# Performance work log

Hardware: AMD Instinct MI355X
Metric: run time of the kernel (lower is better)

## Reference

```python
import jax, jax.numpy as jnp
import numpy as np
import math

DIM = 1024
NUM_HEADS = 16
HEAD_DIM = DIM // NUM_HEADS
EPS = 1e-6
DILATED = 2
WINDOW = 2  # window_size init arg; actual window = L * WINDOW per side


def setup_inputs() -> dict:
    key = jax.random.key(0)
    ks = jax.random.split(key, 14)
    B, S = 1, 8704
    x = jax.random.normal(ks[0], (B, S, DIM), jnp.float32)
    ang = jax.random.uniform(ks[1], (S, HEAD_DIM // 2), jnp.float32, -jnp.pi, jnp.pi)
    freqs_cos = jnp.cos(ang)
    freqs_sin = jnp.sin(ang)
    def lin(k):
        return 0.02 * jax.random.normal(k, (DIM, DIM), jnp.float32)
    def bias(k):
        return 0.01 * jax.random.normal(k, (DIM,), jnp.float32)
    return {
        'x': x, 'freqs_cos': freqs_cos, 'freqs_sin': freqs_sin,
        'wq': lin(ks[2]), 'bq': bias(ks[3]),
        'wk': lin(ks[4]), 'bk': bias(ks[5]),
        'wv': lin(ks[6]), 'bv': bias(ks[7]),
        'wo': lin(ks[8]), 'bo': bias(ks[9]),
        'gq': 1.0 + 0.02 * jax.random.normal(ks[10], (DIM,), jnp.float32),
        'gk': 1.0 + 0.02 * jax.random.normal(ks[11], (DIM,), jnp.float32),
        'f': 34, 'L': 256,
    }


def rmsnorm(h, g):
    return h * jax.lax.rsqrt(jnp.mean(h * h, axis=-1, keepdims=True) + EPS) * g


def rope(h, cos, sin):
    # h: [B,S,D] viewed as interleaved complex pairs per head, rotated by unit freqs
    B, S, D = h.shape
    hp = h.reshape(B, S, NUM_HEADS, HEAD_DIM // 2, 2)
    a, b = hp[..., 0], hp[..., 1]
    c = cos[None, :, None, :]
    s = sin[None, :, None, :]
    ra = a * c - b * s
    rb = a * s + b * c
    return jnp.stack([ra, rb], axis=-1).reshape(B, S, D)


def windowed_attention(q, k, v, w):
    # sliding-window attention: query i attends keys j with |i-j| <= w (inclusive)
    B, S, D = q.shape
    H, hd = NUM_HEADS, HEAD_DIM
    def heads(t):
        return t.reshape(B, S, H, hd).transpose(0, 2, 1, 3)  # [B,H,S,hd]
    qh, kh, vh = heads(q), heads(k), heads(v)
    C = w  # block size == window -> only 3 neighbor key blocks per query block
    pad = (-S) % C
    Sp = S + pad
    nb = Sp // C
    def blocks(t):
        return jnp.pad(t, ((0, 0), (0, 0), (0, pad), (0, 0))).reshape(B, H, nb, C, hd)
    qb = blocks(qh)
    def win(t):
        tb = jnp.pad(blocks(t), ((0, 0), (0, 0), (1, 1), (0, 0), (0, 0)))
        return jnp.concatenate([tb[:, :, i:i + nb] for i in range(3)], axis=3)  # [B,H,nb,3C,hd]
    kw_, vw_ = win(kh), win(vh)
    scores = jnp.einsum('bhnqd,bhnkd->bhnqk', qb, kw_) * (1.0 / math.sqrt(hd))
    qi = jnp.arange(nb)[:, None, None] * C + jnp.arange(C)[None, :, None]      # [nb,C,1]
    kj = (jnp.arange(nb)[:, None, None] - 1) * C + jnp.arange(3 * C)[None, None, :]  # [nb,1,3C]
    valid = (kj >= 0) & (kj < S) & (qi - kj <= w) & (kj - qi <= w)
    scores = jnp.where(valid, scores, -1e9)
    p = jax.nn.softmax(scores, axis=-1)
    o = jnp.einsum('bhnqk,bhnkd->bhnqd', p, vw_)
    return o.reshape(B, H, Sp, hd)[:, :, :S].transpose(0, 2, 1, 3).reshape(B, S, D)


def reference(x, freqs_cos, freqs_sin, wq, bq, wk, bk, wv, bv, wo, bo, gq, gk, f, L):
    B, S, D = x.shape
    q = rope(rmsnorm(x @ wq + bq, gq), freqs_cos, freqs_sin)
    k = rope(rmsnorm(x @ wk + bk, gk), freqs_cos, freqs_sin)
    v = x @ wv + bv
    w = L * WINDOW
    use_dilated = DILATED > 1 and S // (DILATED * L) > 1
    if use_dilated:
        blk = DILATED * L
        pad_len = blk - S % blk  # == blk when S % blk == 0 (faithful to torch code)
        Sp = S + pad_len
        n = Sp // blk
        def padd(t):
            return jnp.pad(t, ((0, 0), (0, pad_len), (0, 0)))
        def dil(t):
            # 'b (n d l) c -> (b d) (n l) c'
            return t.reshape(B, n, DILATED, L, D).transpose(0, 2, 1, 3, 4).reshape(B * DILATED, n * L, D)
        q, k, v = dil(padd(q)), dil(padd(k)), dil(padd(v))
    o = windowed_attention(q, k, v, w)
    out = o @ wo + bo
    if use_dilated:
        # '(b d) (n l) c -> b (n d l) c', then drop pad
        out = out.reshape(B, DILATED, n, L, D).transpose(0, 2, 1, 3, 4).reshape(B, n * DILATED * L, D)
        out = out[:, :S]
    return out
```

## Files before the change

kernel.cpp:

```cpp
#include <hip/hip_runtime.h>
#include <hip/hip_bf16.h>
#include <stdint.h>

#define DIM 1024
#define NH 16
#define HD 64
#define S_ORIG 8704
#define WIN 512

typedef __attribute__((ext_vector_type(8))) short short8;
typedef __attribute__((ext_vector_type(4))) float f32x4;

__device__ __forceinline__ float bf2f(unsigned short u) {
    return __uint_as_float(((unsigned int)u) << 16);
}
__device__ __forceinline__ unsigned short f2bf(float f) {
    unsigned int x = __float_as_uint(f);
    unsigned int r = x + 0x7fffu + ((x >> 16) & 1u);
    return (unsigned short)(r >> 16);
}
__device__ __forceinline__ unsigned int pkbf(float a, float b) {
    unsigned int ua = (__float_as_uint(a) + 0x8000u) >> 16;
    unsigned int ub = (__float_as_uint(b) + 0x8000u) & 0xffff0000u;
    return ua | ub;
}

#define GLD_LDS(gptr, lptr) \
    __builtin_amdgcn_global_load_lds((const __attribute__((address_space(1))) void*)(gptr), \
                                     (__attribute__((address_space(3))) void*)(lptr), 16, 0, 0)

__global__ __launch_bounds__(256) void cvt_x(const float* __restrict__ x,
                                             unsigned short* __restrict__ xb) {
    int i = (blockIdx.x * 256 + threadIdx.x) * 4;
    float4 v = *(const float4*)(x + i);
    ushort4 o;
    o.x = f2bf(v.x); o.y = f2bf(v.y); o.z = f2bf(v.z); o.w = f2bf(v.w);
    *(ushort4*)(xb + i) = o;
}

__global__ __launch_bounds__(256) void transpose_w(const float* __restrict__ w0,
                                                   const float* __restrict__ w1,
                                                   const float* __restrict__ w2,
                                                   const float* __restrict__ w3,
                                                   unsigned short* __restrict__ wt) {
    __shared__ float ts[64][65];
    const int z = blockIdx.z;
    const float* w = z == 0 ? w0 : z == 1 ? w1 : z == 2 ? w2 : w3;
    unsigned short* o = wt + (size_t)z * DIM * DIM;
    const int kb = blockIdx.x * 64, nb = blockIdx.y * 64;
    const int t = threadIdx.x, c = t & 63, r4 = t >> 6;
#pragma unroll
    for (int rr = 0; rr < 16; rr++) {
        int row = rr * 4 + r4;
        ts[row][c] = w[(size_t)(kb + row) * DIM + nb + c];
    }
    __syncthreads();
#pragma unroll
    for (int rr = 0; rr < 16; rr++) {
        int nl = rr * 4 + r4;
        o[(size_t)(nb + nl) * DIM + kb + c] = f2bf(ts[c][nl]);
    }
}

template <int OUTF32>
__global__ __launch_bounds__(256) void gemm_bf16(const unsigned short* __restrict__ A,
                                                 const unsigned short* __restrict__ Bt,
                                                 const float* __restrict__ b0,
                                                 const float* __restrict__ b1,
                                                 const float* __restrict__ b2,
                                                 void* __restrict__ Cout) {
    __shared__ __align__(16) unsigned short As[128 * 32];
    __shared__ __align__(16) unsigned short Bs[128 * 32];
    const int z = blockIdx.z;
    const unsigned short* B = Bt + (size_t)z * DIM * DIM;
    const float* bias = z == 0 ? b0 : (z == 1 ? b1 : b2);
    const int m0 = blockIdx.y * 128, n0 = blockIdx.x * 128;
    const int tid = threadIdx.x;
    const int lane = tid & 63, wv = tid >> 6;
    const int wr = wv >> 1, wc = wv & 1;
    const int quad = lane >> 4, r = lane & 15;

    f32x4 acc[4][4];
#pragma unroll
    for (int i = 0; i < 4; i++)
#pragma unroll
        for (int j = 0; j < 4; j++)
#pragma unroll
            for (int t4 = 0; t4 < 4; t4++) acc[i][j][t4] = 0.0f;

    const unsigned short* a_base = A + (size_t)m0 * DIM;
    const unsigned short* b_base = B + (size_t)n0 * DIM;
    const int c0 = wv * 128 + lane;
    const int r0 = c0 >> 2, o0 = (c0 & 3) * 8;
    const int c1 = c0 + 64;
    const int r1 = c1 >> 2, o1 = (c1 & 3) * 8;
    unsigned short* lA0 = &As[(size_t)(wv * 128) * 8];
    unsigned short* lA1 = &As[(size_t)(wv * 128 + 64) * 8];
    unsigned short* lB0 = &Bs[(size_t)(wv * 128) * 8];
    unsigned short* lB1 = &Bs[(size_t)(wv * 128 + 64) * 8];

    for (int k0 = 0; k0 < DIM; k0 += 32) {
        __syncthreads();
        GLD_LDS(a_base + (size_t)r0 * DIM + k0 + o0, lA0);
        GLD_LDS(a_base + (size_t)r1 * DIM + k0 + o1, lA1);
        GLD_LDS(b_base + (size_t)r0 * DIM + k0 + o0, lB0);
        GLD_LDS(b_base + (size_t)r1 * DIM + k0 + o1, lB1);
        __syncthreads();
        short8 af[4], bfr[4];
#pragma unroll
        for (int i = 0; i < 4; i++)
            af[i] = *(const short8*)&As[(wr * 64 + i * 16 + r) * 32 + quad * 8];
#pragma unroll
        for (int j = 0; j < 4; j++)
            bfr[j] = *(const short8*)&Bs[(wc * 64 + j * 16 + r) * 32 + quad * 8];
#pragma unroll
        for (int i = 0; i < 4; i++)
#pragma unroll
            for (int j = 0; j < 4; j++)
                acc[i][j] = __builtin_amdgcn_mfma_f32_16x16x32_bf16(af[i], bfr[j], acc[i][j], 0, 0, 0);
    }

#pragma unroll
    for (int i = 0; i < 4; i++) {
        const int row = m0 + wr * 64 + i * 16 + quad * 4;
#pragma unroll
        for (int j = 0; j < 4; j++) {
            const int col = n0 + wc * 64 + j * 16 + r;
            const float bvl = bias[col];
#pragma unroll
            for (int t4 = 0; t4 < 4; t4++) {
                float vv = acc[i][j][t4] + bvl;
                if (OUTF32) {
                    ((float*)Cout)[(size_t)(row + t4) * DIM + col] = vv;
                } else {
                    ((unsigned short*)Cout)[(size_t)z * S_ORIG * DIM + (size_t)(row + t4) * DIM + col] = f2bf(vv);
                }
            }
        }
    }
}

__global__ __launch_bounds__(256) void norm_rope(unsigned short* __restrict__ hq,
                                                 unsigned short* __restrict__ hk,
                                                 const float* __restrict__ gq,
                                                 const float* __restrict__ gk,
                                                 const float* __restrict__ fcos,
                                                 const float* __restrict__ fsin) {
    const int srow = blockIdx.x;
    const int z = blockIdx.y;
    unsigned short* h = z == 0 ? hq : hk;
    const float* g = z == 0 ? gq : gk;
    const int tid = threadIdx.x;
    const int base = tid * 4;
    unsigned short* hp = h + (size_t)srow * DIM;

    ushort4 raw = *(const ushort4*)(hp + base);
    float v0 = bf2f(raw.x), v1 = bf2f(raw.y), v2 = bf2f(raw.z), v3 = bf2f(raw.w);
    float ss = v0 * v0 + v1 * v1 + v2 * v2 + v3 * v3;
#pragma unroll
    for (int off = 1; off < 64; off <<= 1) ss += __shfl_xor(ss, off, 64);
    __shared__ float red[4];
    if ((tid & 63) == 0) red[tid >> 6] = ss;
    __syncthreads();
    ss = red[0] + red[1] + red[2] + red[3];
    const float rinv = rsqrtf(ss * (1.0f / DIM) + 1e-6f);

    float4 gv = *(const float4*)(g + base);
    v0 *= rinv * gv.x;
    v1 *= rinv * gv.y;
    v2 *= rinv * gv.z;
    v3 *= rinv * gv.w;

    const int i0 = (base & 63) >> 1;
    float2 cs = *(const float2*)(fcos + (size_t)srow * 32 + i0);
    float2 sn = *(const float2*)(fsin + (size_t)srow * 32 + i0);
    float ra0 = v0 * cs.x - v1 * sn.x;
    float rb0 = v0 * sn.x + v1 * cs.x;
    float ra1 = v2 * cs.y - v3 * sn.y;
    float rb1 = v2 * sn.y + v3 * cs.y;
    ushort4 o;
    o.x = f2bf(ra0); o.y = f2bf(rb0); o.z = f2bf(ra1); o.w = f2bf(rb1);
    *(ushort4*)(hp + base) = o;
}

__global__ __launch_bounds__(256) void attn(const unsigned short* __restrict__ qkv,
                                            unsigned short* __restrict__ ob) {
    __shared__ __align__(16) unsigned short Ks[64 * 72];
    __shared__ __align__(16) unsigned short Vt[64 * 72];
    __shared__ __align__(16) unsigned short Ps[4][16 * 72];

    const int head = blockIdx.x >> 1;
    const int d = blockIdx.x & 1;
    const int qt = blockIdx.y;
    const int tid = threadIdx.x;
    const int lane = tid & 63, wv = tid >> 6;
    const int quad = lane >> 4, r16 = lane & 15;

    const unsigned short* qb = qkv;
    const unsigned short* kb = qkv + (size_t)S_ORIG * DIM;
    const unsigned short* vb = qkv + (size_t)2 * S_ORIG * DIM;

    const int qi = qt * 64 + wv * 16 + r16;
    const int og_q = ((qi >> 8) << 9) + d * 256 + (qi & 255);
    short8 qf[2];
    {
        const unsigned short* qrow = qb + (size_t)og_q * DIM + head * HD + quad * 8;
#pragma unroll
        for (int c = 0; c < 2; c++) {
            union { int4 i4; unsigned short u[8]; short8 s8; } in, outv;
            in.i4 = *(const int4*)(qrow + c * 32);
#pragma unroll
            for (int j = 0; j < 8; j++) outv.u[j] = f2bf(bf2f(in.u[j]) * 0.125f);
            qf[c] = outv.s8;
        }
    }

    f32x4 oacc[4];
    float lsum = 0.0f;
#pragma unroll
    for (int nt = 0; nt < 4; nt++)
#pragma unroll
        for (int rr = 0; rr < 4; rr++) oacc[nt][rr] = 0.0f;

    const int kt_lo = (qt - 8 > 0) ? (qt - 8) : 0;
    const int kt_hi = (qt + 8 < 67) ? (qt + 8) : 67;

    const int st_row0 = tid >> 3, st_ch = (tid & 7) * 8;
    const int vt_kk = (tid & 31) * 2, vt_d0 = (tid >> 5) * 8;

    for (int kt = kt_lo; kt <= kt_hi; kt++) {
        const int kbase = kt * 64;
        __syncthreads();

#pragma unroll
        for (int half = 0; half < 2; half++) {
            const int row = st_row0 + half * 32;
            const int kj = kbase + row;
            const int ok = ((kj >> 8) << 9) + d * 256 + (kj & 255);
            *(int4*)&Ks[row * 72 + st_ch] = *(const int4*)(kb + (size_t)ok * DIM + head * HD + st_ch);
        }
        {
            const int kj0 = kbase + vt_kk;
            const int ok0 = ((kj0 >> 8) << 9) + d * 256 + (kj0 & 255);
            union { int4 i4; unsigned short u[8]; } a0, a1;
            a0.i4 = *(const int4*)(vb + (size_t)ok0 * DIM + head * HD + vt_d0);
            a1.i4 = *(const int4*)(vb + (size_t)(ok0 + 1) * DIM + head * HD + vt_d0);
#pragma unroll
            for (int i = 0; i < 8; i++) {
                unsigned int pack = (unsigned int)a0.u[i] | ((unsigned int)a1.u[i] << 16);
                *(unsigned int*)&Vt[(vt_d0 + i) * 72 + vt_kk] = pack;
            }
        }
        __syncthreads();

        f32x4 sv[4];
#pragma unroll
        for (int nt = 0; nt < 4; nt++) {
            short8 k0f = *(const short8*)&Ks[(nt * 16 + r16) * 72 + quad * 8];
            short8 k1f = *(const short8*)&Ks[(nt * 16 + r16) * 72 + 32 + quad * 8];
            f32x4 a = {0.0f, 0.0f, 0.0f, 0.0f};
            a = __builtin_amdgcn_mfma_f32_16x16x32_bf16(k0f, qf[0], a, 0, 0, 0);
            a = __builtin_amdgcn_mfma_f32_16x16x32_bf16(k1f, qf[1], a, 0, 0, 0);
            sv[nt] = a;
        }

        const bool edge = (kt == qt - 8) || (kt == qt + 8);
        unsigned short* pw = &Ps[wv][0];
#pragma unroll
        for (int nt = 0; nt < 4; nt++) {
            float p[4];
#pragma unroll
            for (int rr = 0; rr < 4; rr++) {
                float e = __expf(sv[nt][rr]);
                if (edge) {
                    const int kj = kbase + nt * 16 + quad * 4 + rr;
                    const int dl = qi - kj;
                    if (dl > WIN || dl < -WIN) e = 0.0f;
                }
                p[rr] = e;
            }
            lsum += (p[0] + p[1]) + (p[2] + p[3]);
            uint2 pk;
            pk.x = pkbf(p[0], p[1]);
            pk.y = pkbf(p[2], p[3]);
            *(uint2*)&pw[r16 * 72 + nt * 16 + quad * 4] = pk;
        }
        __asm__ volatile("s_waitcnt lgkmcnt(0)" ::: "memory");

        short8 pf0 = *(const short8*)&pw[r16 * 72 + quad * 8];
        short8 pf1 = *(const short8*)&pw[r16 * 72 + 32 + quad * 8];
#pragma unroll
        for (int nt = 0; nt < 4; nt++) {
            short8 v0f = *(const short8*)&Vt[(nt * 16 + r16) * 72 + quad * 8];
            short8 v1f = *(const short8*)&Vt[(nt * 16 + r16) * 72 + 32 + quad * 8];
            oacc[nt] = __builtin_amdgcn_mfma_f32_16x16x32_bf16(v0f, pf0, oacc[nt], 0, 0, 0);
            oacc[nt] = __builtin_amdgcn_mfma_f32_16x16x32_bf16(v1f, pf1, oacc[nt], 0, 0, 0);
        }
    }

    lsum += __shfl_xor(lsum, 16, 64);
    lsum += __shfl_xor(lsum, 32, 64);
    {
        const int cnt = (qi + WIN < 4607 ? qi + WIN : 4607) - 4351;
        if (cnt > 0) lsum += (float)cnt;
    }
    const float linv = 1.0f / lsum;

#pragma unroll
    for (int nt = 0; nt < 4; nt++) {
        ushort4 o;
        o.x = f2bf(oacc[nt][0] * linv);
        o.y = f2bf(oacc[nt][1] * linv);
        o.z = f2bf(oacc[nt][2] * linv);
        o.w = f2bf(oacc[nt][3] * linv);
        *(ushort4*)&ob[(size_t)og_q * DIM + head * HD + nt * 16 + quad * 4] = o;
    }
}

extern "C" void kernel_launch(void* const* d_in, const int* in_sizes, int n_in,
                              void* d_out, int out_size, void* d_ws, size_t ws_size,
                              hipStream_t stream) {
    const float* x    = (const float*)d_in[0];
    const float* fcos = (const float*)d_in[1];
    const float* fsin = (const float*)d_in[2];
    const float* wq   = (const float*)d_in[3];
    const float* bq   = (const float*)d_in[4];
    const float* wk   = (const float*)d_in[5];
    const float* bk   = (const float*)d_in[6];
    const float* wv   = (const float*)d_in[7];
    const float* bv   = (const float*)d_in[8];
    const float* wo   = (const float*)d_in[9];
    const float* bo   = (const float*)d_in[10];
    const float* gq   = (const float*)d_in[11];
    const float* gk   = (const float*)d_in[12];

    char* ws = (char*)d_ws;
    unsigned short* xb = (unsigned short*)(ws);
    unsigned short* wt = (unsigned short*)(ws + 17825792);
    unsigned short* h  = (unsigned short*)(ws + 26214400);
    unsigned short* ob = (unsigned short*)(ws + 79691776);
    float* outp = (float*)d_out;

    cvt_x<<<8704, 256, 0, stream>>>(x, xb);
    transpose_w<<<dim3(16, 16, 4), 256, 0, stream>>>(wq, wk, wv, wo, wt);
    gemm_bf16<0><<<dim3(8, 68, 3), 256, 0, stream>>>(xb, wt, bq, bk, bv, (void*)h);
    norm_rope<<<dim3(8704, 2), 256, 0, stream>>>(h, h + (size_t)S_ORIG * DIM, gq, gk, fcos, fsin);
    attn<<<dim3(32, 68), 256, 0, stream>>>(h, ob);
    gemm_bf16<1><<<dim3(8, 68, 1), 256, 0, stream>>>(ob, wt + (size_t)3 * DIM * DIM, bo, bo, bo, (void*)outp);
}
```

Baseline: 334.0 us.

## Widen GEMM K-tile with swizzled LDS, merge prep kernels, warp-per-row norm, exp2 softmax

The GEMM now stages 64-wide K tiles with an XOR-swizzled LDS layout, which halves the barrier count and avoids bank conflicts on fragment reads. The bf16 conversion and weight transpose are merged into one launch. norm_rope now uses one wavefront per row with 16-byte accesses and no shared-memory reduction. Attention folds log2(e) into the query scale and uses exp2f instead of __expf. Rounding the scaled query to bf16 with a non-power-of-two factor adds a small precision change.

```diff
diff --git a/kernel.cpp b/kernel.cpp
--- a/kernel.cpp
+++ b/kernel.cpp
@@ -29,26 +29,31 @@
     __builtin_amdgcn_global_load_lds((const __attribute__((address_space(1))) void*)(gptr), \
                                      (__attribute__((address_space(3))) void*)(lptr), 16, 0, 0)
 
-__global__ __launch_bounds__(256) void cvt_x(const float* __restrict__ x,
-                                             unsigned short* __restrict__ xb) {
-    int i = (blockIdx.x * 256 + threadIdx.x) * 4;
-    float4 v = *(const float4*)(x + i);
-    ushort4 o;
-    o.x = f2bf(v.x); o.y = f2bf(v.y); o.z = f2bf(v.z); o.w = f2bf(v.w);
-    *(ushort4*)(xb + i) = o;
-}
-
-__global__ __launch_bounds__(256) void transpose_w(const float* __restrict__ w0,
-                                                   const float* __restrict__ w1,
-                                                   const float* __restrict__ w2,
-                                                   const float* __restrict__ w3,
-                                                   unsigned short* __restrict__ wt) {
+__global__ __launch_bounds__(256) void prep(const float* __restrict__ x,
+                                            unsigned short* __restrict__ xb,
+                                            const float* __restrict__ w0,
+                                            const float* __restrict__ w1,
+                                            const float* __restrict__ w2,
+                                            const float* __restrict__ w3,
+                                            unsigned short* __restrict__ wt) {
     __shared__ float ts[64][65];
-    const int z = blockIdx.z;
+    const int bx = blockIdx.x;
+    const int t = threadIdx.x;
+    if (bx < 8704) {
+        int i = (bx * 256 + t) * 4;
+        float4 v = *(const float4*)(x + i);
+        ushort4 o;
+        o.x = f2bf(v.x); o.y = f2bf(v.y); o.z = f2bf(v.z); o.w = f2bf(v.w);
+        *(ushort4*)(xb + i) = o;
+        return;
+    }
+    const int b = bx - 8704;
+    const int z = b >> 8;
+    const int rem = b & 255;
+    const int kb = (rem >> 4) * 64, nb = (rem & 15) * 64;
     const float* w = z == 0 ? w0 : z == 1 ? w1 : z == 2 ? w2 : w3;
     unsigned short* o = wt + (size_t)z * DIM * DIM;
-    const int kb = blockIdx.x * 64, nb = blockIdx.y * 64;
-    const int t = threadIdx.x, c = t & 63, r4 = t >> 6;
+    const int c = t & 63, r4 = t >> 6;
 #pragma unroll
     for (int rr = 0; rr < 16; rr++) {
         int row = rr * 4 + r4;
@@ -69,8 +74,8 @@
                                                  const float* __restrict__ b1,
                                                  const float* __restrict__ b2,
                                                  void* __restrict__ Cout) {
-    __shared__ __align__(16) unsigned short As[128 * 32];
-    __shared__ __align__(16) unsigned short Bs[128 * 32];
+    __shared__ __align__(16) unsigned short As[128 * 64];
+    __shared__ __align__(16) unsigned short Bs[128 * 64];
     const int z = blockIdx.z;
     const unsigned short* B = Bt + (size_t)z * DIM * DIM;
     const float* bias = z == 0 ? b0 : (z == 1 ? b1 : b2);
@@ -90,34 +95,43 @@
 
     const unsigned short* a_base = A + (size_t)m0 * DIM;
     const unsigned short* b_base = B + (size_t)n0 * DIM;
-    const int c0 = wv * 128 + lane;
-    const int r0 = c0 >> 2, o0 = (c0 & 3) * 8;
-    const int c1 = c0 + 64;
-    const int r1 = c1 >> 2, o1 = (c1 & 3) * 8;
-    unsigned short* lA0 = &As[(size_t)(wv * 128) * 8];
-    unsigned short* lA1 = &As[(size_t)(wv * 128 + 64) * 8];
-    unsigned short* lB0 = &Bs[(size_t)(wv * 128) * 8];
-    unsigned short* lB1 = &Bs[(size_t)(wv * 128 + 64) * 8];
-
-    for (int k0 = 0; k0 < DIM; k0 += 32) {
+    int st_row[4], st_gc[4];
+#pragma unroll
+    for (int i = 0; i < 4; i++) {
+        const int c = wv * 256 + i * 64 + lane;
+        st_row[i] = c >> 3;
+        st_gc[i] = ((c & 7) ^ (st_row[i] & 7)) * 8;
+    }
+
+    for (int k0 = 0; k0 < DIM; k0 += 64) {
         __syncthreads();
-        GLD_LDS(a_base + (size_t)r0 * DIM + k0 + o0, lA0);
-        GLD_LDS(a_base + (size_t)r1 * DIM + k0 + o1, lA1);
-        GLD_LDS(b_base + (size_t)r0 * DIM + k0 + o0, lB0);
-        GLD_LDS(b_base + (size_t)r1 * DIM + k0 + o1, lB1);
+#pragma unroll
+        for (int i = 0; i < 4; i++) {
+            GLD_LDS(a_base + (size_t)st_row[i] * DIM + k0 + st_gc[i], &As[(wv * 256 + i * 64) * 8]);
+            GLD_LDS(b_base + (size_t)st_row[i] * DIM + k0 + st_gc[i], &Bs[(wv * 256 + i * 64) * 8]);
+        }
         __syncthreads();
-        short8 af[4], bfr[4];
-#pragma unroll
-        for (int i = 0; i < 4; i++)
-            af[i] = *(const short8*)&As[(wr * 64 + i * 16 + r) * 32 + quad * 8];
-#pragma unroll
-        for (int j = 0; j < 4; j++)
-            bfr[j] = *(const short8*)&Bs[(wc * 64 + j * 16 + r) * 32 + quad * 8];
-#pragma unroll
-        for (int i = 0; i < 4; i++)
-#pragma unroll
-            for (int j = 0; j < 4; j++)
-                acc[i][j] = __builtin_amdgcn_mfma_f32_16x16x32_bf16(af[i], bfr[j], acc[i][j], 0, 0, 0);
+#pragma unroll
+        for (int kh = 0; kh < 2; kh++) {
+            short8 af[4], bfr[4];
+#pragma unroll
+            for (int i = 0; i < 4; i++) {
+                const int row = wr * 64 + i * 16 + r;
+                const int pc = ((quad + 4 * kh) ^ (row & 7)) * 8;
+                af[i] = *(const short8*)&As[row * 64 + pc];
+            }
+#pragma unroll
+            for (int j = 0; j < 4; j++) {
+                const int row = wc * 64 + j * 16 + r;
+                const int pc = ((quad + 4 * kh) ^ (row & 7)) * 8;
+                bfr[j] = *(const short8*)&Bs[row * 64 + pc];
+            }
+#pragma unroll
+            for (int i = 0; i < 4; i++)
+#pragma unroll
+                for (int j = 0; j < 4; j++)
+                    acc[i][j] = __builtin_amdgcn_mfma_f32_16x16x32_bf16(af[i], bfr[j], acc[i][j], 0, 0, 0);
+        }
     }
 
 #pragma unroll
@@ -146,41 +160,53 @@
                                                  const float* __restrict__ gk,
                                                  const float* __restrict__ fcos,
                                                  const float* __restrict__ fsin) {
-    const int srow = blockIdx.x;
     const int z = blockIdx.y;
     unsigned short* h = z == 0 ? hq : hk;
     const float* g = z == 0 ? gq : gk;
-    const int tid = threadIdx.x;
-    const int base = tid * 4;
+    const int w = threadIdx.x >> 6, lane = threadIdx.x & 63;
+    const int srow = blockIdx.x * 4 + w;
     unsigned short* hp = h + (size_t)srow * DIM;
-
-    ushort4 raw = *(const ushort4*)(hp + base);
-    float v0 = bf2f(raw.x), v1 = bf2f(raw.y), v2 = bf2f(raw.z), v3 = bf2f(raw.w);
-    float ss = v0 * v0 + v1 * v1 + v2 * v2 + v3 * v3;
+    const int p0 = lane * 8, p1 = 512 + lane * 8;
+
+    union { int4 i4; unsigned short u[8]; } r0, r1, o0, o1;
+    r0.i4 = *(const int4*)(hp + p0);
+    r1.i4 = *(const int4*)(hp + p1);
+    float v[16];
+#pragma unroll
+    for (int j = 0; j < 8; j++) { v[j] = bf2f(r0.u[j]); v[8 + j] = bf2f(r1.u[j]); }
+
+    float ss = 0.0f;
+#pragma unroll
+    for (int j = 0; j < 16; j++) ss += v[j] * v[j];
 #pragma unroll
     for (int off = 1; off < 64; off <<= 1) ss += __shfl_xor(ss, off, 64);
-    __shared__ float red[4];
-    if ((tid & 63) == 0) red[tid >> 6] = ss;
-    __syncthreads();
-    ss = red[0] + red[1] + red[2] + red[3];
     const float rinv = rsqrtf(ss * (1.0f / DIM) + 1e-6f);
 
-    float4 gv = *(const float4*)(g + base);
-    v0 *= rinv * gv.x;
-    v1 *= rinv * gv.y;
-    v2 *= rinv * gv.z;
-    v3 *= rinv * gv.w;
-
-    const int i0 = (base & 63) >> 1;
-    float2 cs = *(const float2*)(fcos + (size_t)srow * 32 + i0);
-    float2 sn = *(const float2*)(fsin + (size_t)srow * 32 + i0);
-    float ra0 = v0 * cs.x - v1 * sn.x;
-    float rb0 = v0 * sn.x + v1 * cs.x;
-    float ra1 = v2 * cs.y - v3 * sn.y;
-    float rb1 = v2 * sn.y + v3 * cs.y;
-    ushort4 o;
-    o.x = f2bf(ra0); o.y = f2bf(rb0); o.z = f2bf(ra1); o.w = f2bf(rb1);
-    *(ushort4*)(hp + base) = o;
+    float4 ga = *(const float4*)(g + p0), gb = *(const float4*)(g + p0 + 4);
+    float4 gc = *(const float4*)(g + p1), gd = *(const float4*)(g + p1 + 4);
+    const float* gg[4] = {&ga.x, &gb.x, &gc.x, &gd.x};
+#pragma unroll
+    for (int q4 = 0; q4 < 4; q4++)
+#pragma unroll
+        for (int j = 0; j < 4; j++) v[q4 * 4 + j] *= rinv * gg[q4][j];
+
+    const int i0 = (p0 & 63) >> 1;
+    float4 cs = *(const float4*)(fcos + (size_t)srow * 32 + i0);
+    float4 sn = *(const float4*)(fsin + (size_t)srow * 32 + i0);
+    const float* cp = &cs.x;
+    const float* sp = &sn.x;
+#pragma unroll
+    for (int seg = 0; seg < 2; seg++) {
+        unsigned short* uo = seg == 0 ? o0.u : o1.u;
+#pragma unroll
+        for (int pr = 0; pr < 4; pr++) {
+            const float a = v[seg * 8 + pr * 2], b = v[seg * 8 + pr * 2 + 1];
+            uo[pr * 2]     = f2bf(a * cp[pr] - b * sp[pr]);
+            uo[pr * 2 + 1] = f2bf(a * sp[pr] + b * cp[pr]);
+        }
+    }
+    *(int4*)(hp + p0) = o0.i4;
+    *(int4*)(hp + p1) = o1.i4;
 }
 
 __global__ __launch_bounds__(256) void attn(const unsigned short* __restrict__ qkv,
@@ -210,7 +236,7 @@
             union { int4 i4; unsigned short u[8]; short8 s8; } in, outv;
             in.i4 = *(const int4*)(qrow + c * 32);
 #pragma unroll
-            for (int j = 0; j < 8; j++) outv.u[j] = f2bf(bf2f(in.u[j]) * 0.125f);
+            for (int j = 0; j < 8; j++) outv.u[j] = f2bf(bf2f(in.u[j]) * 0.18033688f);
             qf[c] = outv.s8;
         }
     }
@@ -271,7 +297,7 @@
             float p[4];
 #pragma unroll
             for (int rr = 0; rr < 4; rr++) {
-                float e = __expf(sv[nt][rr]);
+                float e = exp2f(sv[nt][rr]);
                 if (edge) {
                     const int kj = kbase + nt * 16 + quad * 4 + rr;
                     const int dl = qi - kj;
@@ -341,10 +367,9 @@
     unsigned short* ob = (unsigned short*)(ws + 79691776);
     float* outp = (float*)d_out;
 
-    cvt_x<<<8704, 256, 0, stream>>>(x, xb);
-    transpose_w<<<dim3(16, 16, 4), 256, 0, stream>>>(wq, wk, wv, wo, wt);
+    prep<<<9728, 256, 0, stream>>>(x, xb, wq, wk, wv, wo, wt);
     gemm_bf16<0><<<dim3(8, 68, 3), 256, 0, stream>>>(xb, wt, bq, bk, bv, (void*)h);
-    norm_rope<<<dim3(8704, 2), 256, 0, stream>>>(h, h + (size_t)S_ORIG * DIM, gq, gk, fcos, fsin);
+    norm_rope<<<dim3(2176, 2), 256, 0, stream>>>(h, h + (size_t)S_ORIG * DIM, gq, gk, fcos, fsin);
     attn<<<dim3(32, 68), 256, 0, stream>>>(h, ob);
     gemm_bf16<1><<<dim3(8, 68, 1), 256, 0, stream>>>(ob, wt + (size_t)3 * DIM * DIM, bo, bo, bo, (void*)outp);
 }
```

Result: no change. 339.9 us (+1.8%).
